# Kernel optimization log

Measured on AMD Instinct MI355X. Metric: run time of the kernel, lower is better.

## Reference

```python
import jax, jax.numpy as jnp
import numpy as np

N = 50000      # total batched graph nodes (both ASTs of all examples)
E = 30000      # edges per edge type
T = 8          # num edge types (no master node, no sibling edges)
H = 128        # gnn hidden = change_vector_dim // 2
TAG = 32       # change-tag embed size
CONTENT = H - TAG
VOCAB = 20000  # rows of token/content encoding table
B = 64         # num examples
STEPS = (3, 3) # layer_time_steps


def setup_inputs() -> dict:
    key = jax.random.key(0)
    ks = jax.random.split(key, 22)
    s = 0.05
    inp = {}
    inp["node_content_ids"] = jax.random.randint(ks[0], (N,), 0, VOCAB)
    inp["node_tag_ids"] = jax.random.randint(ks[1], (N,), 0, 4)
    inp["edge_src"] = jax.random.randint(ks[2], (T, E), 0, N)
    inp["edge_tgt"] = jax.random.randint(ks[3], (T, E), 0, N)
    inp["node2example"] = jnp.sort(jax.random.randint(ks[4], (N,), 0, B))
    inp["content_table"] = jax.random.normal(ks[5], (VOCAB, CONTENT)) * s
    inp["tag_embedding"] = jax.random.normal(ks[6], (4, TAG)) * s
    inp["msg_W"] = jax.random.normal(ks[7], (2, T, H, H)) * s
    inp["msg_b"] = jax.random.normal(ks[8], (2, T, H)) * s
    inp["gru0_Wih"] = jax.random.normal(ks[9], (H, 3 * H)) * s
    inp["gru0_Whh"] = jax.random.normal(ks[10], (H, 3 * H)) * s
    inp["gru0_bih"] = jax.random.normal(ks[11], (3 * H,)) * s
    inp["gru0_bhh"] = jax.random.normal(ks[12], (3 * H,)) * s
    inp["gru1_Wih"] = jax.random.normal(ks[13], (2 * H, 3 * H)) * s  # layer 1 gets residual concat -> 2H input
    inp["gru1_Whh"] = jax.random.normal(ks[14], (H, 3 * H)) * s
    inp["gru1_bih"] = jax.random.normal(ks[15], (3 * H,)) * s
    inp["gru1_bhh"] = jax.random.normal(ks[16], (3 * H,)) * s
    inp["r1_w"] = jax.random.normal(ks[17], (H,)) * s
    inp["r1_b"] = jax.random.normal(ks[18], ()) * s
    inp["r2_w"] = jax.random.normal(ks[19], (H,)) * s
    inp["r2_b"] = jax.random.normal(ks[20], ()) * s
    return inp


def _gru(x, h, Wih, Whh, bih, bhh):
    # PyTorch GRUCell gate order: r, z, n
    gi = x @ Wih + bih
    gh = h @ Whh + bhh
    i_r, i_z, i_n = jnp.split(gi, 3, axis=-1)
    h_r, h_z, h_n = jnp.split(gh, 3, axis=-1)
    r = jax.nn.sigmoid(i_r + h_r)
    z = jax.nn.sigmoid(i_z + h_z)
    n = jnp.tanh(i_n + r * h_n)
    return (1.0 - z) * n + z * h


def reference(node_content_ids, node_tag_ids, edge_src, edge_tgt, node2example,
              content_table, tag_embedding, msg_W, msg_b,
              gru0_Wih, gru0_Whh, gru0_bih, gru0_bhh,
              gru1_Wih, gru1_Whh, gru1_bih, gru1_bhh,
              r1_w, r1_b, r2_w, r2_b):
    # init node embeddings: [token/content encoding || change-tag embedding] -> [N, H]
    init = jnp.concatenate([content_table[node_content_ids],
                            tag_embedding[node_tag_ids]], axis=-1)
    states = init
    layer_out = []
    for layer, steps in enumerate(STEPS):
        for _ in range(steps):
            src_states = states[edge_src]                                   # [T,E,H] gather
            msgs = jnp.einsum('teh,thd->ted', src_states, msg_W[layer]) \
                   + msg_b[layer][:, None, :]                               # per-edge-type linear
            agg = jnp.zeros_like(states).at[edge_tgt].add(msgs)             # scatter-add to targets
            if layer == 1:
                # residual_connections={1:[0]}: concat initial states with incoming messages
                x = jnp.concatenate([init, agg], axis=-1)
                states = _gru(x, states, gru1_Wih, gru1_Whh, gru1_bih, gru1_bhh)
            else:
                states = _gru(agg, states, gru0_Wih, gru0_Whh, gru0_bih, gru0_bhh)
        layer_out.append(states)
    s1, s2 = layer_out
    # gated scalar readout per layer, pooled per example, concatenated -> [B, 2H]
    g1 = jax.nn.sigmoid(s1 @ r1_w + r1_b)[:, None]
    g2 = jax.nn.sigmoid(s2 @ r2_w + r2_b)[:, None]
    pooled1 = jax.ops.segment_sum(g1 * s1, node2example, num_segments=B)
    pooled2 = jax.ops.segment_sum(g2 * s2, node2example, num_segments=B)
    return jnp.concatenate([pooled1, pooled2], axis=-1)
```

## Files before the change

### kernel.cpp

```cpp
#include <hip/hip_runtime.h>
#include <hip/hip_bf16.h>

#define NN 50000
#define NE 30000
#define NT 8
#define HH 128
#define NB 64
#define CONT 96
#define TPB 16
#define EDGES (NT * NE)
#define SBLK 512
#define SNB ((NN + SBLK - 1) / SBLK)
#define RCH 8
#define NTILE (NN / 16)
#define GBLK ((NTILE + 3) / 4)

typedef __attribute__((ext_vector_type(8))) short short8;
typedef __attribute__((ext_vector_type(4))) float f32x4;

__device__ __forceinline__ float sigm(float x) { return 1.f / (1.f + __expf(-x)); }
__device__ __forceinline__ unsigned short bfbits(float x) {
  __hip_bfloat16 b = __float2bfloat16(x);
  return *(unsigned short*)&b;
}

__global__ __launch_bounds__(256) void init_kernel(
    const int* __restrict__ cid, const int* __restrict__ tg,
    const float* __restrict__ ctab, const float* __restrict__ ttab,
    __hip_bfloat16* __restrict__ sbf, __hip_bfloat16* __restrict__ ibf)
{
  int i = blockIdx.x * 256 + threadIdx.x;
  if (i >= NN * HH) return;
  int n = i >> 7, d = i & 127;
  float v;
  if (d < CONT) v = ctab[(size_t)cid[n] * CONT + d];
  else          v = ttab[(size_t)tg[n] * 32 + (d - CONT)];
  __hip_bfloat16 b = __float2bfloat16(v);
  sbf[i] = b;
  ibf[i] = b;
}

__global__ __launch_bounds__(256) void hist_kernel(
    const int* __restrict__ etgt, int* __restrict__ cnt)
{
  int i = blockIdx.x * 256 + threadIdx.x;
  if (i >= EDGES) return;
  atomicAdd(&cnt[etgt[i]], 1);
}

__global__ __launch_bounds__(SBLK) void scanA_kernel(
    const int* __restrict__ cnt, int* __restrict__ row_ptr, int* __restrict__ bsum)
{
  __shared__ int sm[SBLK];
  const int tid = threadIdx.x;
  const int i = blockIdx.x * SBLK + tid;
  int v = (i < NN) ? cnt[i] : 0;
  sm[tid] = v;
  __syncthreads();
  for (int off = 1; off < SBLK; off <<= 1) {
    int t = (tid >= off) ? sm[tid - off] : 0;
    __syncthreads();
    sm[tid] += t;
    __syncthreads();
  }
  if (i < NN) row_ptr[i] = sm[tid] - v;
  if (tid == SBLK - 1) bsum[blockIdx.x] = sm[tid];
}

__global__ __launch_bounds__(128) void scanB_kernel(
    const int* __restrict__ bsum, int* __restrict__ boff, int* __restrict__ row_ptr)
{
  __shared__ int sm[128];
  const int tid = threadIdx.x;
  int v = (tid < SNB) ? bsum[tid] : 0;
  sm[tid] = v;
  __syncthreads();
  for (int off = 1; off < 128; off <<= 1) {
    int t = (tid >= off) ? sm[tid - off] : 0;
    __syncthreads();
    sm[tid] += t;
    __syncthreads();
  }
  if (tid < SNB) boff[tid] = sm[tid] - v;
  if (tid == 127) row_ptr[NN] = sm[127];
}

__global__ __launch_bounds__(SBLK) void scanC_kernel(
    int* __restrict__ row_ptr, int* __restrict__ cnt2, const int* __restrict__ boff)
{
  int i = blockIdx.x * SBLK + threadIdx.x;
  if (i >= NN) return;
  int r = row_ptr[i] + boff[blockIdx.x];
  row_ptr[i] = r;
  cnt2[i] = r;
}

__global__ __launch_bounds__(256) void scatter_kernel(
    const int* __restrict__ etgt, int* __restrict__ cnt2, int* __restrict__ perm)
{
  int i = blockIdx.x * 256 + threadIdx.x;
  if (i >= EDGES) return;
  perm[i] = atomicAdd(&cnt2[etgt[i]], 1);
}

__global__ __launch_bounds__(128) void exbound_kernel(
    const int* __restrict__ n2e, int* __restrict__ ebnd)
{
  int ex = threadIdx.x;
  if (ex > NB) return;
  int lo = 0, hi = NN;
  while (lo < hi) { int mid = (lo + hi) >> 1; if (n2e[mid] < ex) lo = mid + 1; else hi = mid; }
  ebnd[ex] = lo;
}

__device__ __forceinline__ void gru_swz_one(
    const float* __restrict__ W, __hip_bfloat16* __restrict__ out, int KSL, int mode, int i)
{
  int j = i & 7, lane = (i >> 3) & 63, kk = (i >> 9) % KSL, nt = i / (KSL * 512);
  int hi = lane >> 4, lo = lane & 15;
  int p = kk * 32 + hi * 8 + j;
  int k;
  if (mode == 0)      k = p;
  else if (mode == 1) k = (p & 7) * 16 + (p >> 3);
  else                k = (p < 128) ? p : 128 + ((p - 128) & 7) * 16 + ((p - 128) >> 3);
  out[i] = __float2bfloat16(W[(size_t)k * 384 + nt * 16 + lo]);
}

__global__ __launch_bounds__(256) void wswz_all_kernel(
    const float* __restrict__ msgW, __hip_bfloat16* __restrict__ wswz,
    const float* __restrict__ g0Wih, __hip_bfloat16* __restrict__ w0ih,
    const float* __restrict__ g0Whh, __hip_bfloat16* __restrict__ w0hh,
    const float* __restrict__ g1Wih, __hip_bfloat16* __restrict__ w1ih,
    const float* __restrict__ g1Whh, __hip_bfloat16* __restrict__ w1hh)
{
  int i = blockIdx.x * 256 + threadIdx.x;
  if (i < 262144) {
    int j = i & 7, lane = (i >> 3) & 63, kk = (i >> 9) & 3, nt = (i >> 11) & 7, lt = i >> 14;
    int hi = lane >> 4, lo = lane & 15;
    int k = kk * 32 + hi * 8 + j;
    wswz[i] = __float2bfloat16(msgW[((size_t)lt * HH + k) * HH + nt * 16 + lo]);
    return;
  }
  i -= 262144;
  if (i < 49152)  { gru_swz_one(g0Wih, w0ih, 4, 1, i); return; }
  i -= 49152;
  if (i < 49152)  { gru_swz_one(g0Whh, w0hh, 4, 0, i); return; }
  i -= 49152;
  if (i < 98304)  { gru_swz_one(g1Wih, w1ih, 8, 2, i); return; }
  i -= 98304;
  if (i < 49152)  { gru_swz_one(g1Whh, w1hh, 4, 0, i); return; }
}

__global__ __launch_bounds__(256) void msg_mfma_kernel(
    const __hip_bfloat16* __restrict__ sbf, const int* __restrict__ esrc,
    const int* __restrict__ perm, const __hip_bfloat16* __restrict__ wswz,
    const float* __restrict__ ball, __hip_bfloat16* __restrict__ msgs, int layer)
{
  __shared__ short8 Wl[8 * 4 * 64];
  const int t = blockIdx.y;
  {
    const float4* wg = (const float4*)(wswz + (size_t)(layer * NT + t) * 16384);
    float4* wl = (float4*)Wl;
    for (int i = threadIdx.x; i < 2048; i += 256) wl[i] = wg[i];
  }
  const int lane = threadIdx.x & 63;
  const int wv   = threadIdx.x >> 6;
  const int hi = lane >> 4, lo = lane & 15;
  float bias_v[8];
#pragma unroll
  for (int nt = 0; nt < 8; ++nt)
    bias_v[nt] = ball[(layer * NT + t) * HH + nt * 16 + lo];
  __syncthreads();

  const int tile_end = min((int)(blockIdx.x + 1) * TPB, NE / 16);
  for (int tile = blockIdx.x * TPB + wv; tile < tile_end; tile += 4) {
    const int e0 = tile * 16;
    const int src = esrc[t * NE + e0 + lo];
    const short* srow = (const short*)(sbf + (size_t)src * HH);
    short8 a[4];
#pragma unroll
    for (int kk = 0; kk < 4; ++kk)
      a[kk] = *(const short8*)(srow + kk * 32 + hi * 8);
    int slot[4];
#pragma unroll
    for (int r = 0; r < 4; ++r) slot[r] = perm[t * NE + e0 + hi * 4 + r];
    f32x4 acc[8];
#pragma unroll
    for (int nt = 0; nt < 8; ++nt) acc[nt] = (f32x4){0.f, 0.f, 0.f, 0.f};
#pragma unroll
    for (int nt = 0; nt < 8; ++nt)
#pragma unroll
      for (int kk = 0; kk < 4; ++kk)
        acc[nt] = __builtin_amdgcn_mfma_f32_16x16x32_bf16(
            a[kk], Wl[(nt * 4 + kk) * 64 + lane], acc[nt], 0, 0, 0);
#pragma unroll
    for (int r = 0; r < 4; ++r) {
      short8 m;
#pragma unroll
      for (int nt = 0; nt < 8; ++nt)
        ((unsigned short*)&m)[nt] = bfbits(acc[nt][r] + bias_v[nt]);
      *(short8*)((short*)msgs + (size_t)slot[r] * HH + lo * 8) = m;
    }
  }
}

__global__ __launch_bounds__(256) void reduce_kernel(
    const __hip_bfloat16* __restrict__ msgs, const int* __restrict__ row_ptr,
    __hip_bfloat16* __restrict__ agg)
{
  const int lane = threadIdx.x & 63;
  const int n = blockIdx.x * 4 + (threadIdx.x >> 6);
  if (n >= NN) return;
  const int b = row_ptr[n], e = row_ptr[n + 1];
  float a0 = 0.f, a1 = 0.f;
  for (int i = b; i < e; ++i) {
    unsigned int v = *(const unsigned int*)((const short*)msgs + (size_t)i * HH + lane * 2);
    a0 += __uint_as_float(v << 16);
    a1 += __uint_as_float(v & 0xffff0000u);
  }
  unsigned int o = ((unsigned int)bfbits(a1) << 16) | bfbits(a0);
  *(unsigned int*)((short*)agg + (size_t)n * HH + lane * 2) = o;
}

template <int KSL>
__global__ __launch_bounds__(256) void gru_mfma_kernel(
    const __hip_bfloat16* __restrict__ agg,
    const __hip_bfloat16* __restrict__ ibf,
    const __hip_bfloat16* __restrict__ hbf,
    const __hip_bfloat16* __restrict__ Wih_s,
    const __hip_bfloat16* __restrict__ Whh_s,
    const float* __restrict__ bih, const float* __restrict__ bhh,
    __hip_bfloat16* __restrict__ sbf_out)
{
  const int lane = threadIdx.x & 63;
  const int wv   = threadIdx.x >> 6;
  const int dtg  = blockIdx.x / GBLK;
  const int tile = (blockIdx.x % GBLK) * 4 + wv;
  if (tile >= NTILE) return;
  const int nb = tile * 16;
  const int hi = lane >> 4, lo = lane & 15;

  short8 ax[KSL], ah[4];
  {
    const short* arow = (const short*)(agg + (size_t)(nb + lo) * HH);
    const short* hrow = (const short*)(hbf + (size_t)(nb + lo) * HH);
    if (KSL == 8) {
      const short* irow = (const short*)(ibf + (size_t)(nb + lo) * HH);
#pragma unroll
      for (int kk = 0; kk < 4; ++kk) {
        ax[kk]     = *(const short8*)(irow + kk * 32 + hi * 8);
        ax[kk + 4] = *(const short8*)(arow + kk * 32 + hi * 8);
      }
    } else {
#pragma unroll
      for (int kk = 0; kk < 4; ++kk)
        ax[kk] = *(const short8*)(arow + kk * 32 + hi * 8);
    }
#pragma unroll
    for (int kk = 0; kk < 4; ++kk)
      ah[kk] = *(const short8*)(hrow + kk * 32 + hi * 8);
  }

  const short8* __restrict__ Bih = (const short8*)Wih_s;
  const short8* __restrict__ Bhh = (const short8*)Whh_s;

#pragma unroll
  for (int d2 = 0; d2 < 2; ++d2) {
    const int dt = dtg * 2 + d2;
    f32x4 gi[3], gh[3];
#pragma unroll
    for (int g = 0; g < 3; ++g) {
      gi[g] = (f32x4){0.f, 0.f, 0.f, 0.f};
      gh[g] = (f32x4){0.f, 0.f, 0.f, 0.f};
    }
#pragma unroll
    for (int kk = 0; kk < KSL; ++kk)
#pragma unroll
      for (int g = 0; g < 3; ++g)
        gi[g] = __builtin_amdgcn_mfma_f32_16x16x32_bf16(
            ax[kk], Bih[((size_t)(dt + 8 * g) * KSL + kk) * 64 + lane], gi[g], 0, 0, 0);
#pragma unroll
    for (int kk = 0; kk < 4; ++kk)
#pragma unroll
      for (int g = 0; g < 3; ++g)
        gh[g] = __builtin_amdgcn_mfma_f32_16x16x32_bf16(
            ah[kk], Bhh[((size_t)(dt + 8 * g) * 4 + kk) * 64 + lane], gh[g], 0, 0, 0);
    const int c = dt * 16 + lo;
    const float bir = bih[c], biz = bih[c + 128], bin = bih[c + 256];
    const float bhr = bhh[c], bhz = bhh[c + 128], bhn = bhh[c + 256];
#pragma unroll
    for (int r = 0; r < 4; ++r) {
      const int node = nb + hi * 4 + r;
      const float rg = sigm(gi[0][r] + bir + gh[0][r] + bhr);
      const float zg = sigm(gi[1][r] + biz + gh[1][r] + bhz);
      const float ng = tanhf(gi[2][r] + bin + rg * (gh[2][r] + bhn));
      const float hc = __bfloat162float(hbf[(size_t)node * HH + c]);
      sbf_out[(size_t)node * HH + c] = __float2bfloat16((1.f - zg) * ng + zg * hc);
    }
  }
}

__global__ __launch_bounds__(256) void readout_kernel(
    const __hip_bfloat16* __restrict__ sbf, const int* __restrict__ ebnd,
    const float* __restrict__ rw, const float* __restrict__ rb,
    float* __restrict__ out, int coff)
{
  __shared__ float sm[4][128];
  const int ex = blockIdx.x / RCH, ch = blockIdx.x % RCH;
  const int s = ebnd[ex], e = ebnd[ex + 1];
  const int lane = threadIdx.x & 63;
  const int wv   = threadIdx.x >> 6;
  const float w0 = rw[2 * lane], w1 = rw[2 * lane + 1], rbv = rb[0];
  float a0 = 0.f, a1 = 0.f;
  for (int n = s + ch * 4 + wv; n < e; n += 4 * RCH) {
    unsigned int v = *(const unsigned int*)((const short*)sbf + (size_t)n * HH + lane * 2);
    const float s0 = __uint_as_float(v << 16);
    const float s1 = __uint_as_float(v & 0xffff0000u);
    float p = s0 * w0 + s1 * w1;
#pragma unroll
    for (int o = 32; o; o >>= 1) p += __shfl_xor(p, o, 64);
    const float g = sigm(p + rbv);
    a0 += g * s0;
    a1 += g * s1;
  }
  sm[wv][2 * lane] = a0;
  sm[wv][2 * lane + 1] = a1;
  __syncthreads();
  if (wv == 0) {
    const int c0 = 2 * lane, c1 = 2 * lane + 1;
    float v0 = sm[0][c0] + sm[1][c0] + sm[2][c0] + sm[3][c0];
    float v1 = sm[0][c1] + sm[1][c1] + sm[2][c1] + sm[3][c1];
    atomicAdd(&out[(size_t)ex * (2 * HH) + coff + c0], v0);
    atomicAdd(&out[(size_t)ex * (2 * HH) + coff + c1], v1);
  }
}

extern "C" void kernel_launch(void* const* d_in, const int* in_sizes, int n_in,
                              void* d_out, int out_size, void* d_ws, size_t ws_size,
                              hipStream_t stream)
{
  const int*   cid   = (const int*)d_in[0];
  const int*   tg    = (const int*)d_in[1];
  const int*   esrc  = (const int*)d_in[2];
  const int*   etgt  = (const int*)d_in[3];
  const int*   n2e   = (const int*)d_in[4];
  const float* ctab  = (const float*)d_in[5];
  const float* ttab  = (const float*)d_in[6];
  const float* msgW  = (const float*)d_in[7];
  const float* msgb  = (const float*)d_in[8];
  const float* g0Wih = (const float*)d_in[9];
  const float* g0Whh = (const float*)d_in[10];
  const float* g0bih = (const float*)d_in[11];
  const float* g0bhh = (const float*)d_in[12];
  const float* g1Wih = (const float*)d_in[13];
  const float* g1Whh = (const float*)d_in[14];
  const float* g1bih = (const float*)d_in[15];
  const float* g1bhh = (const float*)d_in[16];
  const float* r1w   = (const float*)d_in[17];
  const float* r1b   = (const float*)d_in[18];
  const float* r2w   = (const float*)d_in[19];
  const float* r2b   = (const float*)d_in[20];

  float* out = (float*)d_out;
  __hip_bfloat16* sb0  = (__hip_bfloat16*)d_ws;
  __hip_bfloat16* sb1  = sb0 + (size_t)NN * HH;
  __hip_bfloat16* ibf  = sb1 + (size_t)NN * HH;
  __hip_bfloat16* agg  = ibf + (size_t)NN * HH;
  __hip_bfloat16* msgs = agg + (size_t)NN * HH;
  __hip_bfloat16* wswz = msgs + (size_t)EDGES * HH;
  __hip_bfloat16* w0ih = wswz + 262144;
  __hip_bfloat16* w0hh = w0ih + 24 * 4 * 512;
  __hip_bfloat16* w1ih = w0hh + 24 * 4 * 512;
  __hip_bfloat16* w1hh = w1ih + 24 * 8 * 512;
  int* row_ptr = (int*)(w1hh + 24 * 4 * 512);
  int* cnt     = row_ptr + NN + 1;
  int* cnt2    = cnt + NN;
  int* perm    = cnt2 + NN;
  int* bsum    = perm + EDGES;
  int* boff    = bsum + SNB;
  int* ebnd    = boff + SNB;

  hipMemsetAsync(d_out, 0, (size_t)NB * 2 * HH * sizeof(float), stream);
  hipMemsetAsync(cnt, 0, (size_t)NN * sizeof(int), stream);
  const int eblocks = (EDGES + 255) / 256;
  hist_kernel<<<eblocks, 256, 0, stream>>>(etgt, cnt);
  scanA_kernel<<<SNB, SBLK, 0, stream>>>(cnt, row_ptr, bsum);
  scanB_kernel<<<1, 128, 0, stream>>>(bsum, boff, row_ptr);
  scanC_kernel<<<SNB, SBLK, 0, stream>>>(row_ptr, cnt2, boff);
  scatter_kernel<<<eblocks, 256, 0, stream>>>(etgt, cnt2, perm);
  exbound_kernel<<<1, 128, 0, stream>>>(n2e, ebnd);

  wswz_all_kernel<<<507904 / 256, 256, 0, stream>>>(msgW, wswz, g0Wih, w0ih, g0Whh, w0hh,
                                                    g1Wih, w1ih, g1Whh, w1hh);
  init_kernel<<<(NN * HH + 255) / 256, 256, 0, stream>>>(cid, tg, ctab, ttab, sb0, ibf);

  dim3 mgrid((NE / 16 + TPB - 1) / TPB, NT);
  const int rblocks = (NN + 3) / 4;
  __hip_bfloat16* cur = sb0;
  __hip_bfloat16* nxt = sb1;
  for (int s = 0; s < 3; ++s) {
    msg_mfma_kernel<<<mgrid, 256, 0, stream>>>(cur, esrc, perm, wswz, msgb, msgs, 0);
    reduce_kernel<<<rblocks, 256, 0, stream>>>(msgs, row_ptr, agg);
    gru_mfma_kernel<4><<<4 * GBLK, 256, 0, stream>>>(agg, ibf, cur, w0ih, w0hh,
                                                     g0bih, g0bhh, nxt);
    __hip_bfloat16* t = cur; cur = nxt; nxt = t;
  }
  readout_kernel<<<NB * RCH, 256, 0, stream>>>(cur, ebnd, r1w, r1b, out, 0);

  for (int s = 0; s < 3; ++s) {
    msg_mfma_kernel<<<mgrid, 256, 0, stream>>>(cur, esrc, perm, wswz, msgb, msgs, 1);
    reduce_kernel<<<rblocks, 256, 0, stream>>>(msgs, row_ptr, agg);
    gru_mfma_kernel<8><<<4 * GBLK, 256, 0, stream>>>(agg, ibf, cur, w1ih, w1hh,
                                                     g1bih, g1bhh, nxt);
    __hip_bfloat16* t = cur; cur = nxt; nxt = t;
  }
  readout_kernel<<<NB * RCH, 256, 0, stream>>>(cur, ebnd, r2w, r2b, out, HH);
}
```

Measured before the change: 716.1 us.

## Stage GRU weights in LDS and process two node tiles per wave

```diff
diff --git a/kernel.cpp b/kernel.cpp
--- a/kernel.cpp
+++ b/kernel.cpp
@@ -13,7 +13,7 @@
 #define SNB ((NN + SBLK - 1) / SBLK)
 #define RCH 8
 #define NTILE (NN / 16)
-#define GBLK ((NTILE + 3) / 4)
+#define NPAIR ((NTILE + 1) / 2)
 
 typedef __attribute__((ext_vector_type(8))) short short8;
 typedef __attribute__((ext_vector_type(4))) float f32x4;
@@ -232,70 +232,115 @@
     const float* __restrict__ bih, const float* __restrict__ bhh,
     __hip_bfloat16* __restrict__ sbf_out)
 {
+  __shared__ short8 BihL[2 * 3 * KSL * 64];
+  __shared__ short8 BhhL[2 * 3 * 4 * 64];
+  const int dtg = blockIdx.y;
+  {
+    const short8* Bih_g = (const short8*)Wih_s;
+    const short8* Bhh_g = (const short8*)Whh_s;
+    for (int i = threadIdx.x; i < 2 * 3 * KSL * 64; i += 256) {
+      int lane_i = i & 63, kk = (i >> 6) % KSL, g = ((i >> 6) / KSL) % 3, d2 = (i >> 6) / (KSL * 3);
+      BihL[i] = Bih_g[((size_t)(dtg * 2 + d2 + 8 * g) * KSL + kk) * 64 + lane_i];
+    }
+    for (int i = threadIdx.x; i < 2 * 3 * 4 * 64; i += 256) {
+      int lane_i = i & 63, kk = (i >> 6) & 3, g = ((i >> 6) >> 2) % 3, d2 = (i >> 6) / 12;
+      BhhL[i] = Bhh_g[((size_t)(dtg * 2 + d2 + 8 * g) * 4 + kk) * 64 + lane_i];
+    }
+  }
   const int lane = threadIdx.x & 63;
   const int wv   = threadIdx.x >> 6;
-  const int dtg  = blockIdx.x / GBLK;
-  const int tile = (blockIdx.x % GBLK) * 4 + wv;
-  if (tile >= NTILE) return;
-  const int nb = tile * 16;
   const int hi = lane >> 4, lo = lane & 15;
-
-  short8 ax[KSL], ah[4];
-  {
+  float birv[2], bizv[2], binv[2], bhrv[2], bhzv[2], bhnv[2];
+#pragma unroll
+  for (int d2 = 0; d2 < 2; ++d2) {
+    const int c = (dtg * 2 + d2) * 16 + lo;
+    birv[d2] = bih[c]; bizv[d2] = bih[c + 128]; binv[d2] = bih[c + 256];
+    bhrv[d2] = bhh[c]; bhzv[d2] = bhh[c + 128]; bhnv[d2] = bhh[c + 256];
+  }
+  __syncthreads();
+
+  const int pt = blockIdx.x * 4 + wv;
+  if (pt >= NPAIR) return;
+  const int t0 = pt * 2;
+  const bool two = (t0 + 1 < NTILE);
+
+  short8 ax[2][KSL], ah[2][4];
+#pragma unroll
+  for (int u = 0; u < 2; ++u) {
+    const int nb = ((u && two) ? t0 + 1 : t0) * 16;
     const short* arow = (const short*)(agg + (size_t)(nb + lo) * HH);
     const short* hrow = (const short*)(hbf + (size_t)(nb + lo) * HH);
     if (KSL == 8) {
       const short* irow = (const short*)(ibf + (size_t)(nb + lo) * HH);
 #pragma unroll
       for (int kk = 0; kk < 4; ++kk) {
-        ax[kk]     = *(const short8*)(irow + kk * 32 + hi * 8);
-        ax[kk + 4] = *(const short8*)(arow + kk * 32 + hi * 8);
+        ax[u][kk]     = *(const short8*)(irow + kk * 32 + hi * 8);
+        ax[u][kk + 4] = *(const short8*)(arow + kk * 32 + hi * 8);
       }
     } else {
 #pragma unroll
-      for (int kk = 0; kk < 4; ++kk)
-        ax[kk] = *(const short8*)(arow + kk * 32 + hi * 8);
+      for (int kk = 0; kk < KSL; ++kk)
+        ax[u][kk] = *(const short8*)(arow + kk * 32 + hi * 8);
     }
 #pragma unroll
     for (int kk = 0; kk < 4; ++kk)
-      ah[kk] = *(const short8*)(hrow + kk * 32 + hi * 8);
-  }
-
-  const short8* __restrict__ Bih = (const short8*)Wih_s;
-  const short8* __restrict__ Bhh = (const short8*)Whh_s;
+      ah[u][kk] = *(const short8*)(hrow + kk * 32 + hi * 8);
+  }
+
+  f32x4 aR[2][2], aZ[2][2], aNi[2][2], aNh[2][2];
+#pragma unroll
+  for (int d2 = 0; d2 < 2; ++d2)
+#pragma unroll
+    for (int u = 0; u < 2; ++u) {
+      aR[d2][u] = (f32x4){0.f, 0.f, 0.f, 0.f};
+      aZ[d2][u] = (f32x4){0.f, 0.f, 0.f, 0.f};
+      aNi[d2][u] = (f32x4){0.f, 0.f, 0.f, 0.f};
+      aNh[d2][u] = (f32x4){0.f, 0.f, 0.f, 0.f};
+    }
 
 #pragma unroll
   for (int d2 = 0; d2 < 2; ++d2) {
-    const int dt = dtg * 2 + d2;
-    f32x4 gi[3], gh[3];
-#pragma unroll
-    for (int g = 0; g < 3; ++g) {
-      gi[g] = (f32x4){0.f, 0.f, 0.f, 0.f};
-      gh[g] = (f32x4){0.f, 0.f, 0.f, 0.f};
-    }
-#pragma unroll
-    for (int kk = 0; kk < KSL; ++kk)
-#pragma unroll
-      for (int g = 0; g < 3; ++g)
-        gi[g] = __builtin_amdgcn_mfma_f32_16x16x32_bf16(
-            ax[kk], Bih[((size_t)(dt + 8 * g) * KSL + kk) * 64 + lane], gi[g], 0, 0, 0);
-#pragma unroll
-    for (int kk = 0; kk < 4; ++kk)
-#pragma unroll
-      for (int g = 0; g < 3; ++g)
-        gh[g] = __builtin_amdgcn_mfma_f32_16x16x32_bf16(
-            ah[kk], Bhh[((size_t)(dt + 8 * g) * 4 + kk) * 64 + lane], gh[g], 0, 0, 0);
-    const int c = dt * 16 + lo;
-    const float bir = bih[c], biz = bih[c + 128], bin = bih[c + 256];
-    const float bhr = bhh[c], bhz = bhh[c + 128], bhn = bhh[c + 256];
-#pragma unroll
-    for (int r = 0; r < 4; ++r) {
-      const int node = nb + hi * 4 + r;
-      const float rg = sigm(gi[0][r] + bir + gh[0][r] + bhr);
-      const float zg = sigm(gi[1][r] + biz + gh[1][r] + bhz);
-      const float ng = tanhf(gi[2][r] + bin + rg * (gh[2][r] + bhn));
-      const float hc = __bfloat162float(hbf[(size_t)node * HH + c]);
-      sbf_out[(size_t)node * HH + c] = __float2bfloat16((1.f - zg) * ng + zg * hc);
+#pragma unroll
+    for (int kk = 0; kk < KSL; ++kk) {
+      short8 br = BihL[((d2 * 3 + 0) * KSL + kk) * 64 + lane];
+      short8 bz = BihL[((d2 * 3 + 1) * KSL + kk) * 64 + lane];
+      short8 bn = BihL[((d2 * 3 + 2) * KSL + kk) * 64 + lane];
+#pragma unroll
+      for (int u = 0; u < 2; ++u) {
+        aR[d2][u]  = __builtin_amdgcn_mfma_f32_16x16x32_bf16(ax[u][kk], br, aR[d2][u], 0, 0, 0);
+        aZ[d2][u]  = __builtin_amdgcn_mfma_f32_16x16x32_bf16(ax[u][kk], bz, aZ[d2][u], 0, 0, 0);
+        aNi[d2][u] = __builtin_amdgcn_mfma_f32_16x16x32_bf16(ax[u][kk], bn, aNi[d2][u], 0, 0, 0);
+      }
+    }
+#pragma unroll
+    for (int kk = 0; kk < 4; ++kk) {
+      short8 br = BhhL[((d2 * 3 + 0) * 4 + kk) * 64 + lane];
+      short8 bz = BhhL[((d2 * 3 + 1) * 4 + kk) * 64 + lane];
+      short8 bn = BhhL[((d2 * 3 + 2) * 4 + kk) * 64 + lane];
+#pragma unroll
+      for (int u = 0; u < 2; ++u) {
+        aR[d2][u]  = __builtin_amdgcn_mfma_f32_16x16x32_bf16(ah[u][kk], br, aR[d2][u], 0, 0, 0);
+        aZ[d2][u]  = __builtin_amdgcn_mfma_f32_16x16x32_bf16(ah[u][kk], bz, aZ[d2][u], 0, 0, 0);
+        aNh[d2][u] = __builtin_amdgcn_mfma_f32_16x16x32_bf16(ah[u][kk], bn, aNh[d2][u], 0, 0, 0);
+      }
+    }
+  }
+
+  const int uend = two ? 2 : 1;
+  for (int u = 0; u < uend; ++u) {
+    const int nb = (t0 + u) * 16;
+#pragma unroll
+    for (int d2 = 0; d2 < 2; ++d2) {
+      const int c = (dtg * 2 + d2) * 16 + lo;
+#pragma unroll
+      for (int r = 0; r < 4; ++r) {
+        const int node = nb + hi * 4 + r;
+        const float rg = sigm(aR[d2][u][r] + birv[d2] + bhrv[d2]);
+        const float zg = sigm(aZ[d2][u][r] + bizv[d2] + bhzv[d2]);
+        const float ng = tanhf(aNi[d2][u][r] + binv[d2] + rg * (aNh[d2][u][r] + bhnv[d2]));
+        const float hc = __bfloat162float(hbf[(size_t)node * HH + c]);
+        sbf_out[(size_t)node * HH + c] = __float2bfloat16((1.f - zg) * ng + zg * hc);
+      }
     }
   }
 }
@@ -395,14 +440,15 @@
   init_kernel<<<(NN * HH + 255) / 256, 256, 0, stream>>>(cid, tg, ctab, ttab, sb0, ibf);
 
   dim3 mgrid((NE / 16 + TPB - 1) / TPB, NT);
+  dim3 ggrid((NPAIR + 3) / 4, 4);
   const int rblocks = (NN + 3) / 4;
   __hip_bfloat16* cur = sb0;
   __hip_bfloat16* nxt = sb1;
   for (int s = 0; s < 3; ++s) {
     msg_mfma_kernel<<<mgrid, 256, 0, stream>>>(cur, esrc, perm, wswz, msgb, msgs, 0);
     reduce_kernel<<<rblocks, 256, 0, stream>>>(msgs, row_ptr, agg);
-    gru_mfma_kernel<4><<<4 * GBLK, 256, 0, stream>>>(agg, ibf, cur, w0ih, w0hh,
-                                                     g0bih, g0bhh, nxt);
+    gru_mfma_kernel<4><<<ggrid, 256, 0, stream>>>(agg, ibf, cur, w0ih, w0hh,
+                                                  g0bih, g0bhh, nxt);
     __hip_bfloat16* t = cur; cur = nxt; nxt = t;
   }
   readout_kernel<<<NB * RCH, 256, 0, stream>>>(cur, ebnd, r1w, r1b, out, 0);
@@ -410,8 +456,8 @@
   for (int s = 0; s < 3; ++s) {
     msg_mfma_kernel<<<mgrid, 256, 0, stream>>>(cur, esrc, perm, wswz, msgb, msgs, 1);
     reduce_kernel<<<rblocks, 256, 0, stream>>>(msgs, row_ptr, agg);
-    gru_mfma_kernel<8><<<4 * GBLK, 256, 0, stream>>>(agg, ibf, cur, w1ih, w1hh,
-                                                     g1bih, g1bhh, nxt);
+    gru_mfma_kernel<8><<<ggrid, 256, 0, stream>>>(agg, ibf, cur, w1ih, w1hh,
+                                                  g1bih, g1bhh, nxt);
     __hip_bfloat16* t = cur; cur = nxt; nxt = t;
   }
   readout_kernel<<<NB * RCH, 256, 0, stream>>>(cur, ebnd, r2w, r2b, out, HH);
```

Measured after the change: 644.5 us. -10.0%, faster.
